# Kernel tuning notes

Measured on AMD Instinct MI355X. Metric: run time of the kernel, lower is better.

Reference implementation:

```python
import math
import jax, jax.numpy as jnp
import numpy as np

# ---- module constants (from init_kwargs) ----
B, IN, OUT, NR = 4096, 512, 512, 16
WL_MIN, WL_MAX = 1546.0e-9, 1554.0e-9
WL0 = 0.5 * (WL_MIN + WL_MAX)          # center wavelength
R_UM, NEFF, NG = 30.0, 2.34, 4.2
LOSS_DB_CM, KAPPA = 3.0, 0.2
L = 2.0 * math.pi * (R_UM * 1e-6)      # ring circumference [m]
A_AMP = 10.0 ** (-LOSS_DB_CM * (L * 100.0) / 20.0)  # single-pass amplitude
R_T = math.sqrt(1.0 - KAPPA)           # through-coupling amplitude


def _ring_neffs():
    # per-ring effective index detuning from phase_offsets (as in __init__)
    offsets = jnp.linspace(-math.pi, math.pi, NR, dtype=jnp.float32)
    return jnp.float32(NEFF) + offsets * jnp.float32(WL0 / (2.0 * math.pi * L))  # [NR]


def _evaluate_basis(x):
    # wavelengths driven by (clamped) inputs: [B, IN]
    wl = WL_MIN + 0.5 * (jnp.clip(x, -1.0, 1.0) + 1.0) * (WL_MAX - WL_MIN)
    wl = wl[..., None]                                  # [B, IN, 1]
    neff_r = _ring_neffs()                              # [NR]
    # first-order dispersion around WL0 (waveguide with neff, ng)
    neff_wl = neff_r - (wl - WL0) * (NG - neff_r) / WL0  # [B, IN, NR]
    phi = (2.0 * math.pi * L) * neff_wl / wl            # round-trip phase
    c = jnp.cos(phi)
    # all-pass ring power throughput (analytic transfer function)
    num = A_AMP * A_AMP - 2.0 * R_T * A_AMP * c + R_T * R_T
    den = 1.0 - 2.0 * R_T * A_AMP * c + (R_T * A_AMP) ** 2
    return num / den                                    # [B, IN, NR]


def setup_inputs() -> dict:
    key = jax.random.key(0)
    k1, k2, k3 = jax.random.split(key, 3)
    x = jax.random.normal(k1, (B, IN), dtype=jnp.float32)
    coeffs = jax.random.normal(k2, (IN, OUT, NR), dtype=jnp.float32) * 0.05
    base_weight = jax.random.normal(k3, (IN, OUT), dtype=jnp.float32) * 0.05
    return {"x": x, "coeffs": coeffs, "base_weight": base_weight}


def reference(x, coeffs, base_weight):
    basis = _evaluate_basis(x)                          # [B, IN, NR]
    basis_out = jnp.einsum('bin,ion->bo', basis, coeffs)  # [B, OUT]
    residual = x @ base_weight                          # [B, OUT]
    kl = jnp.zeros((1,), dtype=x.dtype)                 # non-variational path
    return (basis_out + residual, kl)
```

## Files before the change

kernel.cpp:

```cpp
#include <hip/hip_runtime.h>
#include <hip/hip_bf16.h>
#include <cmath>
#include <cstdint>

#define Bsz   4096
#define INsz  512
#define OUTsz 512
#define NRING 16
#define KTOT  8704
#define SPLITK 4
#define NPH   34

using short8 = __attribute__((ext_vector_type(8))) short;
using f32x4  = __attribute__((ext_vector_type(4))) float;

struct RC {
  float Cr[NRING];
  float Snr[NRING];
  float K2, SQ, pad0, pad1;
};

__device__ __forceinline__ unsigned short f2bf(float f) {
  __hip_bfloat16 h = __float2bfloat16(f);
  return *reinterpret_cast<unsigned short*>(&h);
}
__device__ __forceinline__ float fastrcp(float x) {
#if __has_builtin(__builtin_amdgcn_rcpf)
  return __builtin_amdgcn_rcpf(x);
#else
  return 1.0f / x;
#endif
}
__device__ __forceinline__ float fastfract(float x) {
#if __has_builtin(__builtin_amdgcn_fractf)
  return __builtin_amdgcn_fractf(x);
#else
  return x - floorf(x);
#endif
}
__device__ __forceinline__ float cos2pi(float fr) {
#if __has_builtin(__builtin_amdgcn_cosf)
  return __builtin_amdgcn_cosf(fr);
#else
  return __cosf(fr * 6.28318530717958647692f);
#endif
}
__device__ __forceinline__ float sin2pi(float fr) {
#if __has_builtin(__builtin_amdgcn_sinf)
  return __builtin_amdgcn_sinf(fr);
#else
  return __sinf(fr * 6.28318530717958647692f);
#endif
}

__device__ __forceinline__ void gl_lds16(const void* g, void* l) {
  __builtin_amdgcn_global_load_lds(
      (const __attribute__((address_space(1))) void*)g,
      (__attribute__((address_space(3))) void*)l, 16, 0, 0);
}

__global__ __launch_bounds__(512) void pack_b_kernel(
    const float* __restrict__ coeffs, const float* __restrict__ bw,
    unsigned short* __restrict__ Bt, float* __restrict__ bias, float PQ) {
  __shared__ float red[8];
  const int o = blockIdx.x;
  const int i = threadIdx.x;
  const float* cp = coeffs + ((size_t)i * OUTsz + o) * NRING;
  unsigned short* row = Bt + (size_t)o * KTOT + i;
  float s = 0.0f;
#pragma unroll
  for (int j = 0; j < 4; ++j) {
    f32x4 v = *reinterpret_cast<const f32x4*>(cp + j * 4);
#pragma unroll
    for (int e = 0; e < 4; ++e) {
      const int n = j * 4 + e;
      s += v[e];
      row[(size_t)n * INsz] = f2bf(PQ * v[e]);
    }
  }
  row[(size_t)NRING * INsz] = f2bf(bw[(size_t)i * OUTsz + o]);
#pragma unroll
  for (int off = 32; off > 0; off >>= 1) s += __shfl_down(s, off);
  const int w = i >> 6;
  if ((i & 63) == 0) red[w] = s;
  __syncthreads();
  if (i == 0) {
    float t = 0.0f;
#pragma unroll
    for (int k = 0; k < 8; ++k) t += red[k];
    bias[o] = t;
  }
}

__global__ __launch_bounds__(512) void gemm_fused_kernel(
    const float* __restrict__ x, const unsigned short* __restrict__ Bt,
    float* __restrict__ part, RC rc) {
  extern __shared__ char smem[];
  char* smA = smem;
  char* smB = smem + 32768;
  const int tid  = threadIdx.x;
  const int lane = tid & 63;
  const int w    = tid >> 6;
  const int bid  = blockIdx.x;
  const int cbks = bid & 7;
  const int rb   = bid >> 3;
  const int cb   = cbks & 1, ks = cbks >> 1;
  const int brow = rb * 128, bcol = cb * 256;

  const int r  = tid & 127;
  const int q4 = tid >> 7;
  const int wb0 = r * 128 + (((q4 * 2 + 0) ^ (r & 7)) * 16);
  const int wb1 = r * 128 + (((q4 * 2 + 1) ^ (r & 7)) * 16);

  const int cg = (lane & 7) ^ ((lane >> 3) & 7);
  const unsigned short* gb0 = Bt + (size_t)(bcol + w * 8 + (lane >> 3)) * KTOT + cg * 8;

  const int wr = w >> 2, wc = w & 3;
  const int l7 = lane & 7;
  const int rowA = wr * 64 + (lane & 15);
  const int rowB = wc * 64 + (lane & 15);

  float xr[32], cth[32], sth[32];
  const float* gx = x + (size_t)(brow + r) * INsz + ks * 128 + q4 * 16;
#pragma unroll
  for (int h = 0; h < 2; ++h)
#pragma unroll
    for (int j = 0; j < 4; ++j) {
      f32x4 v = *reinterpret_cast<const f32x4*>(gx + h * 64 + j * 4);
#pragma unroll
      for (int e = 0; e < 4; ++e) xr[h * 16 + j * 4 + e] = v[e];
    }
#pragma unroll
  for (int c = 0; c < 32; ++c) {
    float xc = fminf(fmaxf(xr[c], -1.0f), 1.0f);
    float wl = __builtin_fmaf(xc, 4.0e-9f, 1550.0e-9f);
    float hh = rc.K2 * xc * fastrcp(wl);
    float fr = fastfract(hh);
    cth[c] = cos2pi(fr);
    sth[c] = sin2pi(fr);
  }

  auto STAGE = [&](int p) {
    const int is = (p >= 17) ? 1 : 0, n = p - 17 * is;
    const size_t koff = (size_t)(n * 512 + ks * 128 + is * 64);
    char* ldst = smB + (p % 3) * 32768 + w * 1024;
    const unsigned short* src = gb0 + koff;
#pragma unroll
    for (int iss = 0; iss < 4; ++iss)
      gl_lds16(src + (size_t)iss * 64 * KTOT, ldst + iss * 8192);
  };
  auto GENA = [&](int p) {
    const int is = (p >= 17) ? 1 : 0, n = p - 17 * is;
    char* dst = smA + (p & 1) * 16384;
    if (n < NRING) {
      const float Crn = rc.Cr[n], Snn = rc.Snr[n];
#pragma unroll
      for (int g = 0; g < 2; ++g) {
        short8 wv;
#pragma unroll
        for (int e = 0; e < 8; ++e) {
          const int c = is * 16 + g * 8 + e;
          float cph = __builtin_fmaf(cth[c], Crn, sth[c] * Snn);
          wv[e] = (short)f2bf(fastrcp(cph + rc.SQ));
        }
        *reinterpret_cast<short8*>(dst + (g ? wb1 : wb0)) = wv;
      }
    } else {
#pragma unroll
      for (int g = 0; g < 2; ++g) {
        short8 wv;
#pragma unroll
        for (int e = 0; e < 8; ++e) wv[e] = (short)f2bf(xr[is * 16 + g * 8 + e]);
        *reinterpret_cast<short8*>(dst + (g ? wb1 : wb0)) = wv;
      }
    }
  };

  f32x4 acc[4][4];
#pragma unroll
  for (int m = 0; m < 4; ++m)
#pragma unroll
    for (int q = 0; q < 4; ++q) acc[m][q] = (f32x4){0.f, 0.f, 0.f, 0.f};

  STAGE(0); STAGE(1);
  GENA(0);
  asm volatile("s_waitcnt vmcnt(4) lgkmcnt(0)" ::: "memory");
  __builtin_amdgcn_s_barrier();
  __builtin_amdgcn_sched_barrier(0);

#pragma unroll
  for (int p = 0; p < NPH; ++p) {
    if (p + 2 < NPH) STAGE(p + 2);
    const char* bA = smA + (p & 1) * 16384;
    const char* bB = smB + (p % 3) * 32768;
    short8 af[2][4], bfr[2][4];
#pragma unroll
    for (int kk = 0; kk < 2; ++kk) {
      const int oct = (((lane >> 4) + kk * 4) ^ l7) * 16;
#pragma unroll
      for (int m = 0; m < 4; ++m)
        af[kk][m] = *reinterpret_cast<const short8*>(bA + (rowA + m * 16) * 128 + oct);
#pragma unroll
      for (int q = 0; q < 4; ++q)
        bfr[kk][q] = *reinterpret_cast<const short8*>(bB + (rowB + q * 16) * 128 + oct);
    }
    if (p + 1 < NPH) GENA(p + 1);
    __builtin_amdgcn_s_setprio(1);
#pragma unroll
    for (int kk = 0; kk < 2; ++kk)
#pragma unroll
      for (int m = 0; m < 4; ++m)
#pragma unroll
        for (int q = 0; q < 4; ++q)
          acc[m][q] = __builtin_amdgcn_mfma_f32_16x16x32_bf16(af[kk][m], bfr[kk][q], acc[m][q], 0, 0, 0);
    __builtin_amdgcn_s_setprio(0);
    if (p + 1 < NPH) {
      if (p + 2 < NPH) {
        asm volatile("s_waitcnt vmcnt(4) lgkmcnt(0)" ::: "memory");
      } else {
        asm volatile("s_waitcnt vmcnt(0) lgkmcnt(0)" ::: "memory");
      }
      __builtin_amdgcn_s_barrier();
      __builtin_amdgcn_sched_barrier(0);
    }
  }

  float* po = part + (size_t)ks * ((size_t)Bsz * OUTsz);
  const int r0 = brow + wr * 64 + ((lane >> 4) * 4);
  const int c0 = bcol + wc * 64 + (lane & 15);
#pragma unroll
  for (int m = 0; m < 4; ++m)
#pragma unroll
    for (int q = 0; q < 4; ++q)
#pragma unroll
      for (int e = 0; e < 4; ++e)
        po[(size_t)(r0 + m * 16 + e) * OUTsz + (c0 + q * 16)] = acc[m][q][e];
}

__global__ __launch_bounds__(256) void reduce_kernel(
    const f32x4* __restrict__ part, const f32x4* __restrict__ bias,
    float* __restrict__ out) {
  const size_t idx = (size_t)blockIdx.x * 256 + threadIdx.x;
  const size_t stride = (size_t)Bsz * OUTsz / 4;
  f32x4 v = part[idx] + part[idx + stride] + part[idx + 2 * stride] + part[idx + 3 * stride];
  v = v + bias[idx & 127];
  reinterpret_cast<f32x4*>(out)[idx] = v;
  if (idx == 0) out[(size_t)Bsz * OUTsz] = 0.0f;
}

extern "C" void kernel_launch(void* const* d_in, const int* in_sizes, int n_in,
                              void* d_out, int out_size, void* d_ws, size_t ws_size,
                              hipStream_t stream) {
  const float* x      = (const float*)d_in[0];
  const float* coeffs = (const float*)d_in[1];
  const float* bw     = (const float*)d_in[2];
  float* out = (float*)d_out;

  unsigned short* Bt = (unsigned short*)d_ws;
  float* part = (float*)((char*)d_ws + (size_t)OUTsz * KTOT * 2);
  float* bias = (float*)((char*)d_ws + (size_t)OUTsz * KTOT * 2
                                     + (size_t)SPLITK * Bsz * OUTsz * 4);

  RC rc;
  float PQ;
  {
    const double PI  = 3.14159265358979323846;
    const double Lc  = 2.0 * PI * 30.0e-6;
    const double WL0 = 1550.0e-9;
    const double NG  = 4.2;
    const double Aamp = pow(10.0, -3.0 * (Lc * 100.0) / 20.0);
    const double Rt2  = 0.8;
    const double Rt   = sqrt(Rt2);
    for (int rr = 0; rr < NRING; ++rr) {
      double off  = -PI + rr * (2.0 * PI / 15.0);
      double neff = 2.34 + off * WL0 / (2.0 * PI * Lc);
      double rev0 = (Lc / WL0) * neff;
      rc.Cr[rr]  = (float)cos(2.0 * PI * rev0);
      rc.Snr[rr] = (float)(-sin(2.0 * PI * rev0));
    }
    const double qn = -2.0 * Rt * Aamp;
    const double s  = 1.0 + Rt2 * Aamp * Aamp;
    const double P  = -(1.0 - Aamp * Aamp) * (1.0 - Rt2);
    rc.K2 = (float)(-4.0e-9 * Lc * NG / WL0);
    rc.SQ = (float)(s / qn);
    rc.pad0 = rc.pad1 = 0.f;
    PQ = (float)(P / qn);
  }

  hipFuncSetAttribute(reinterpret_cast<const void*>(gemm_fused_kernel),
                      hipFuncAttributeMaxDynamicSharedMemorySize, 131072);

  hipLaunchKernelGGL(pack_b_kernel, dim3(OUTsz), dim3(512), 0, stream,
                     coeffs, bw, Bt, bias, PQ);
  hipLaunchKernelGGL(gemm_fused_kernel, dim3(256), dim3(512), 131072, stream,
                     x, Bt, part, rc);
  hipLaunchKernelGGL(reduce_kernel, dim3((Bsz * OUTsz / 4) / 256), dim3(256), 0, stream,
                     (const f32x4*)part, (const f32x4*)bias, out);
}
```

Measured before the change: 62.25 us.

## Halve GEMM column tile to 128 and double grid size for occupancy

Shrinks each block's output tile from 128x256 to 128x128, so the grid doubles to 512 blocks, B-operand LDS staging halves, and dynamic shared memory drops to 80 KB. Per-thread register use is cut by computing trig values for only half the K columns at a time (the second half at phase 16) and pre-converting x to bf16 once. It also adds a launch-bounds occupancy hint. The intent is more active blocks per CU and better load balance across the 256 CUs. In exchange, every block now regenerates the A-operand basis, so that transcendental work is duplicated across twice as many column blocks.

```diff
diff --git a/kernel.cpp b/kernel.cpp
--- a/kernel.cpp
+++ b/kernel.cpp
@@ -92,7 +92,7 @@
   }
 }
 
-__global__ __launch_bounds__(512) void gemm_fused_kernel(
+__global__ __launch_bounds__(512, 4) void gemm_fused_kernel(
     const float* __restrict__ x, const unsigned short* __restrict__ Bt,
     float* __restrict__ part, RC rc) {
   extern __shared__ char smem[];
@@ -102,10 +102,10 @@
   const int lane = tid & 63;
   const int w    = tid >> 6;
   const int bid  = blockIdx.x;
-  const int cbks = bid & 7;
-  const int rb   = bid >> 3;
-  const int cb   = cbks & 1, ks = cbks >> 1;
-  const int brow = rb * 128, bcol = cb * 256;
+  const int combo = bid & 15;
+  const int rb   = bid >> 4;
+  const int cb   = combo & 3, ks = combo >> 2;
+  const int brow = rb * 128, bcol = cb * 128;
 
   const int r  = tid & 127;
   const int q4 = tid >> 7;
@@ -118,36 +118,43 @@
   const int wr = w >> 2, wc = w & 3;
   const int l7 = lane & 7;
   const int rowA = wr * 64 + (lane & 15);
-  const int rowB = wc * 64 + (lane & 15);
-
-  float xr[32], cth[32], sth[32];
+  const int rowB = wc * 32 + (lane & 15);
+
+  float xf0[16], xf1[16], cth[16], sth[16];
+  short8 xbf0a, xbf0b, xbf1a, xbf1b;
   const float* gx = x + (size_t)(brow + r) * INsz + ks * 128 + q4 * 16;
 #pragma unroll
-  for (int h = 0; h < 2; ++h)
-#pragma unroll
-    for (int j = 0; j < 4; ++j) {
-      f32x4 v = *reinterpret_cast<const f32x4*>(gx + h * 64 + j * 4);
-#pragma unroll
-      for (int e = 0; e < 4; ++e) xr[h * 16 + j * 4 + e] = v[e];
-    }
-#pragma unroll
-  for (int c = 0; c < 32; ++c) {
-    float xc = fminf(fmaxf(xr[c], -1.0f), 1.0f);
-    float wl = __builtin_fmaf(xc, 4.0e-9f, 1550.0e-9f);
-    float hh = rc.K2 * xc * fastrcp(wl);
-    float fr = fastfract(hh);
-    cth[c] = cos2pi(fr);
-    sth[c] = sin2pi(fr);
-  }
+  for (int j = 0; j < 4; ++j) {
+    f32x4 v0 = *reinterpret_cast<const f32x4*>(gx + j * 4);
+    f32x4 v1 = *reinterpret_cast<const f32x4*>(gx + 64 + j * 4);
+#pragma unroll
+    for (int e = 0; e < 4; ++e) { xf0[j * 4 + e] = v0[e]; xf1[j * 4 + e] = v1[e]; }
+  }
+#pragma unroll
+  for (int c = 0; c < 8; ++c) {
+    xbf0a[c] = (short)f2bf(xf0[c]);     xbf0b[c] = (short)f2bf(xf0[c + 8]);
+    xbf1a[c] = (short)f2bf(xf1[c]);     xbf1b[c] = (short)f2bf(xf1[c + 8]);
+  }
+  auto TRIG = [&](const float* xf) {
+#pragma unroll
+    for (int c = 0; c < 16; ++c) {
+      float xc = fminf(fmaxf(xf[c], -1.0f), 1.0f);
+      float wl = __builtin_fmaf(xc, 4.0e-9f, 1550.0e-9f);
+      float hh = rc.K2 * xc * fastrcp(wl);
+      float fr = fastfract(hh);
+      cth[c] = cos2pi(fr);
+      sth[c] = sin2pi(fr);
+    }
+  };
+  TRIG(xf0);
 
   auto STAGE = [&](int p) {
     const int is = (p >= 17) ? 1 : 0, n = p - 17 * is;
     const size_t koff = (size_t)(n * 512 + ks * 128 + is * 64);
-    char* ldst = smB + (p % 3) * 32768 + w * 1024;
+    char* ldst = smB + (p % 3) * 16384 + w * 1024;
     const unsigned short* src = gb0 + koff;
-#pragma unroll
-    for (int iss = 0; iss < 4; ++iss)
-      gl_lds16(src + (size_t)iss * 64 * KTOT, ldst + iss * 8192);
+    gl_lds16(src, ldst);
+    gl_lds16(src + (size_t)64 * KTOT, ldst + 8192);
   };
   auto GENA = [&](int p) {
     const int is = (p >= 17) ? 1 : 0, n = p - 17 * is;
@@ -159,41 +166,36 @@
         short8 wv;
 #pragma unroll
         for (int e = 0; e < 8; ++e) {
-          const int c = is * 16 + g * 8 + e;
-          float cph = __builtin_fmaf(cth[c], Crn, sth[c] * Snn);
+          float cph = __builtin_fmaf(cth[g * 8 + e], Crn, sth[g * 8 + e] * Snn);
           wv[e] = (short)f2bf(fastrcp(cph + rc.SQ));
         }
         *reinterpret_cast<short8*>(dst + (g ? wb1 : wb0)) = wv;
       }
     } else {
-#pragma unroll
-      for (int g = 0; g < 2; ++g) {
-        short8 wv;
-#pragma unroll
-        for (int e = 0; e < 8; ++e) wv[e] = (short)f2bf(xr[is * 16 + g * 8 + e]);
-        *reinterpret_cast<short8*>(dst + (g ? wb1 : wb0)) = wv;
-      }
+      *reinterpret_cast<short8*>(dst + wb0) = is ? xbf1a : xbf0a;
+      *reinterpret_cast<short8*>(dst + wb1) = is ? xbf1b : xbf0b;
     }
   };
 
-  f32x4 acc[4][4];
+  f32x4 acc[4][2];
 #pragma unroll
   for (int m = 0; m < 4; ++m)
 #pragma unroll
-    for (int q = 0; q < 4; ++q) acc[m][q] = (f32x4){0.f, 0.f, 0.f, 0.f};
+    for (int q = 0; q < 2; ++q) acc[m][q] = (f32x4){0.f, 0.f, 0.f, 0.f};
 
   STAGE(0); STAGE(1);
   GENA(0);
-  asm volatile("s_waitcnt vmcnt(4) lgkmcnt(0)" ::: "memory");
+  asm volatile("s_waitcnt vmcnt(2) lgkmcnt(0)" ::: "memory");
   __builtin_amdgcn_s_barrier();
   __builtin_amdgcn_sched_barrier(0);
 
 #pragma unroll
   for (int p = 0; p < NPH; ++p) {
     if (p + 2 < NPH) STAGE(p + 2);
+    if (p == 16) TRIG(xf1);
     const char* bA = smA + (p & 1) * 16384;
-    const char* bB = smB + (p % 3) * 32768;
-    short8 af[2][4], bfr[2][4];
+    const char* bB = smB + (p % 3) * 16384;
+    short8 af[2][4], bfr[2][2];
 #pragma unroll
     for (int kk = 0; kk < 2; ++kk) {
       const int oct = (((lane >> 4) + kk * 4) ^ l7) * 16;
@@ -201,7 +203,7 @@
       for (int m = 0; m < 4; ++m)
         af[kk][m] = *reinterpret_cast<const short8*>(bA + (rowA + m * 16) * 128 + oct);
 #pragma unroll
-      for (int q = 0; q < 4; ++q)
+      for (int q = 0; q < 2; ++q)
         bfr[kk][q] = *reinterpret_cast<const short8*>(bB + (rowB + q * 16) * 128 + oct);
     }
     if (p + 1 < NPH) GENA(p + 1);
@@ -211,12 +213,12 @@
 #pragma unroll
       for (int m = 0; m < 4; ++m)
 #pragma unroll
-        for (int q = 0; q < 4; ++q)
+        for (int q = 0; q < 2; ++q)
           acc[m][q] = __builtin_amdgcn_mfma_f32_16x16x32_bf16(af[kk][m], bfr[kk][q], acc[m][q], 0, 0, 0);
     __builtin_amdgcn_s_setprio(0);
     if (p + 1 < NPH) {
       if (p + 2 < NPH) {
-        asm volatile("s_waitcnt vmcnt(4) lgkmcnt(0)" ::: "memory");
+        asm volatile("s_waitcnt vmcnt(2) lgkmcnt(0)" ::: "memory");
       } else {
         asm volatile("s_waitcnt vmcnt(0) lgkmcnt(0)" ::: "memory");
       }
@@ -227,11 +229,11 @@
 
   float* po = part + (size_t)ks * ((size_t)Bsz * OUTsz);
   const int r0 = brow + wr * 64 + ((lane >> 4) * 4);
-  const int c0 = bcol + wc * 64 + (lane & 15);
+  const int c0 = bcol + wc * 32 + (lane & 15);
 #pragma unroll
   for (int m = 0; m < 4; ++m)
 #pragma unroll
-    for (int q = 0; q < 4; ++q)
+    for (int q = 0; q < 2; ++q)
 #pragma unroll
       for (int e = 0; e < 4; ++e)
         po[(size_t)(r0 + m * 16 + e) * OUTsz + (c0 + q * 16)] = acc[m][q][e];
@@ -288,11 +290,11 @@
   }
 
   hipFuncSetAttribute(reinterpret_cast<const void*>(gemm_fused_kernel),
-                      hipFuncAttributeMaxDynamicSharedMemorySize, 131072);
+                      hipFuncAttributeMaxDynamicSharedMemorySize, 81920);
 
   hipLaunchKernelGGL(pack_b_kernel, dim3(OUTsz), dim3(512), 0, stream,
                      coeffs, bw, Bt, bias, PQ);
-  hipLaunchKernelGGL(gemm_fused_kernel, dim3(256), dim3(512), 131072, stream,
+  hipLaunchKernelGGL(gemm_fused_kernel, dim3(512), dim3(512), 81920, stream,
                      x, Bt, part, rc);
   hipLaunchKernelGGL(reduce_kernel, dim3((Bsz * OUTsz / 4) / 256), dim3(256), 0, stream,
                      (const f32x4*)part, (const f32x4*)bias, out);
```

After: 86.62 us. 39.2% more time.

## Split each phase into two ping-pong MFMA halves with extra barriers and lower register use

Applied to the files above, without the earlier changes.

Each pipeline phase now runs as two half-K sub-steps. Each sub-step loads its LDS fragments, passes a barrier and runs 16 MFMAs, and the A-tile generation and global staging are placed between the halves. Register pressure drops because only 16 cos/sin values are kept live (the second half is recomputed at phase 16), and the bf16 copies of x are precomputed once. The aim is better overlap of MFMA with LDS reads and ALU generation and possibly higher occupancy, at the cost of extra barriers per phase.

```diff
diff --git a/kernel.cpp b/kernel.cpp
--- a/kernel.cpp
+++ b/kernel.cpp
@@ -120,25 +120,33 @@
   const int rowA = wr * 64 + (lane & 15);
   const int rowB = wc * 64 + (lane & 15);
 
-  float xr[32], cth[32], sth[32];
+  float xf0[16], xf1[16], cth[16], sth[16];
+  short8 xbf0a, xbf0b, xbf1a, xbf1b;
   const float* gx = x + (size_t)(brow + r) * INsz + ks * 128 + q4 * 16;
 #pragma unroll
-  for (int h = 0; h < 2; ++h)
-#pragma unroll
-    for (int j = 0; j < 4; ++j) {
-      f32x4 v = *reinterpret_cast<const f32x4*>(gx + h * 64 + j * 4);
-#pragma unroll
-      for (int e = 0; e < 4; ++e) xr[h * 16 + j * 4 + e] = v[e];
-    }
-#pragma unroll
-  for (int c = 0; c < 32; ++c) {
-    float xc = fminf(fmaxf(xr[c], -1.0f), 1.0f);
-    float wl = __builtin_fmaf(xc, 4.0e-9f, 1550.0e-9f);
-    float hh = rc.K2 * xc * fastrcp(wl);
-    float fr = fastfract(hh);
-    cth[c] = cos2pi(fr);
-    sth[c] = sin2pi(fr);
-  }
+  for (int j = 0; j < 4; ++j) {
+    f32x4 v0 = *reinterpret_cast<const f32x4*>(gx + j * 4);
+    f32x4 v1 = *reinterpret_cast<const f32x4*>(gx + 64 + j * 4);
+#pragma unroll
+    for (int e = 0; e < 4; ++e) { xf0[j * 4 + e] = v0[e]; xf1[j * 4 + e] = v1[e]; }
+  }
+#pragma unroll
+  for (int c = 0; c < 8; ++c) {
+    xbf0a[c] = (short)f2bf(xf0[c]);     xbf0b[c] = (short)f2bf(xf0[c + 8]);
+    xbf1a[c] = (short)f2bf(xf1[c]);     xbf1b[c] = (short)f2bf(xf1[c + 8]);
+  }
+  auto TRIG = [&](const float* xf) {
+#pragma unroll
+    for (int c = 0; c < 16; ++c) {
+      float xc = fminf(fmaxf(xf[c], -1.0f), 1.0f);
+      float wl = __builtin_fmaf(xc, 4.0e-9f, 1550.0e-9f);
+      float hh = rc.K2 * xc * fastrcp(wl);
+      float fr = fastfract(hh);
+      cth[c] = cos2pi(fr);
+      sth[c] = sin2pi(fr);
+    }
+  };
+  TRIG(xf0);
 
   auto STAGE = [&](int p) {
     const int is = (p >= 17) ? 1 : 0, n = p - 17 * is;
@@ -159,20 +167,14 @@
         short8 wv;
 #pragma unroll
         for (int e = 0; e < 8; ++e) {
-          const int c = is * 16 + g * 8 + e;
-          float cph = __builtin_fmaf(cth[c], Crn, sth[c] * Snn);
+          float cph = __builtin_fmaf(cth[g * 8 + e], Crn, sth[g * 8 + e] * Snn);
           wv[e] = (short)f2bf(fastrcp(cph + rc.SQ));
         }
         *reinterpret_cast<short8*>(dst + (g ? wb1 : wb0)) = wv;
       }
     } else {
-#pragma unroll
-      for (int g = 0; g < 2; ++g) {
-        short8 wv;
-#pragma unroll
-        for (int e = 0; e < 8; ++e) wv[e] = (short)f2bf(xr[is * 16 + g * 8 + e]);
-        *reinterpret_cast<short8*>(dst + (g ? wb1 : wb0)) = wv;
-      }
+      *reinterpret_cast<short8*>(dst + wb0) = is ? xbf1a : xbf0a;
+      *reinterpret_cast<short8*>(dst + wb1) = is ? xbf1b : xbf0b;
     }
   };
 
@@ -190,35 +192,56 @@
 
 #pragma unroll
   for (int p = 0; p < NPH; ++p) {
-    if (p + 2 < NPH) STAGE(p + 2);
     const char* bA = smA + (p & 1) * 16384;
     const char* bB = smB + (p % 3) * 32768;
-    short8 af[2][4], bfr[2][4];
-#pragma unroll
-    for (int kk = 0; kk < 2; ++kk) {
-      const int oct = (((lane >> 4) + kk * 4) ^ l7) * 16;
+    short8 af[4], bfr[4];
+    {
+      const int oct = ((lane >> 4) ^ l7) * 16;
 #pragma unroll
       for (int m = 0; m < 4; ++m)
-        af[kk][m] = *reinterpret_cast<const short8*>(bA + (rowA + m * 16) * 128 + oct);
+        af[m] = *reinterpret_cast<const short8*>(bA + (rowA + m * 16) * 128 + oct);
 #pragma unroll
       for (int q = 0; q < 4; ++q)
-        bfr[kk][q] = *reinterpret_cast<const short8*>(bB + (rowB + q * 16) * 128 + oct);
-    }
+        bfr[q] = *reinterpret_cast<const short8*>(bB + (rowB + q * 16) * 128 + oct);
+    }
+    if (p + 2 < NPH) STAGE(p + 2);
+    __builtin_amdgcn_s_barrier();
+    asm volatile("s_waitcnt lgkmcnt(0)" ::: "memory");
+    __builtin_amdgcn_sched_barrier(0);
+    __builtin_amdgcn_s_setprio(1);
+#pragma unroll
+    for (int m = 0; m < 4; ++m)
+#pragma unroll
+      for (int q = 0; q < 4; ++q)
+        acc[m][q] = __builtin_amdgcn_mfma_f32_16x16x32_bf16(af[m], bfr[q], acc[m][q], 0, 0, 0);
+    __builtin_amdgcn_s_setprio(0);
+    __builtin_amdgcn_s_barrier();
+    {
+      const int oct = (((lane >> 4) + 4) ^ l7) * 16;
+#pragma unroll
+      for (int m = 0; m < 4; ++m)
+        af[m] = *reinterpret_cast<const short8*>(bA + (rowA + m * 16) * 128 + oct);
+#pragma unroll
+      for (int q = 0; q < 4; ++q)
+        bfr[q] = *reinterpret_cast<const short8*>(bB + (rowB + q * 16) * 128 + oct);
+    }
+    if (p == 16) TRIG(xf1);
     if (p + 1 < NPH) GENA(p + 1);
+    __builtin_amdgcn_s_barrier();
+    asm volatile("s_waitcnt lgkmcnt(0)" ::: "memory");
+    __builtin_amdgcn_sched_barrier(0);
     __builtin_amdgcn_s_setprio(1);
 #pragma unroll
-    for (int kk = 0; kk < 2; ++kk)
-#pragma unroll
-      for (int m = 0; m < 4; ++m)
-#pragma unroll
-        for (int q = 0; q < 4; ++q)
-          acc[m][q] = __builtin_amdgcn_mfma_f32_16x16x32_bf16(af[kk][m], bfr[kk][q], acc[m][q], 0, 0, 0);
+    for (int m = 0; m < 4; ++m)
+#pragma unroll
+      for (int q = 0; q < 4; ++q)
+        acc[m][q] = __builtin_amdgcn_mfma_f32_16x16x32_bf16(af[m], bfr[q], acc[m][q], 0, 0, 0);
     __builtin_amdgcn_s_setprio(0);
     if (p + 1 < NPH) {
       if (p + 2 < NPH) {
-        asm volatile("s_waitcnt vmcnt(4) lgkmcnt(0)" ::: "memory");
+        asm volatile("s_waitcnt vmcnt(4)" ::: "memory");
       } else {
-        asm volatile("s_waitcnt vmcnt(0) lgkmcnt(0)" ::: "memory");
+        asm volatile("s_waitcnt vmcnt(0)" ::: "memory");
       }
       __builtin_amdgcn_s_barrier();
       __builtin_amdgcn_sched_barrier(0);
```

Result: slower. 66.92 us (+7.5%).

## Warp-specialize fused GEMM into producer and MFMA consumer wavefronts

Applied to the files above, without the earlier changes.

Doubles the block to 1024 threads: eight producer waves compute the ring basis tiles into LDS and issue global-to-LDS loads of B, while eight consumer waves only read LDS and run MFMA. The aim is to take the transcendental basis generation and load issue off the MFMA waves' critical path. In exchange each block carries more waves, which raises register and occupancy pressure, and loops are no longer unrolled. Producer and consumer waves also use mixed barrier primitives whose counts must match exactly.

```diff
diff --git a/kernel.cpp b/kernel.cpp
--- a/kernel.cpp
+++ b/kernel.cpp
@@ -92,7 +92,7 @@
   }
 }
 
-__global__ __launch_bounds__(512) void gemm_fused_kernel(
+__global__ __launch_bounds__(1024) void gemm_fused_kernel(
     const float* __restrict__ x, const unsigned short* __restrict__ Bt,
     float* __restrict__ part, RC rc) {
   extern __shared__ char smem[];
@@ -102,139 +102,176 @@
   const int lane = tid & 63;
   const int w    = tid >> 6;
   const int bid  = blockIdx.x;
-  const int cbks = bid & 7;
+  const int combo = bid & 7;
   const int rb   = bid >> 3;
-  const int cb   = cbks & 1, ks = cbks >> 1;
+  const int cb   = combo & 1, ks = combo >> 1;
   const int brow = rb * 128, bcol = cb * 256;
 
-  const int r  = tid & 127;
-  const int q4 = tid >> 7;
-  const int wb0 = r * 128 + (((q4 * 2 + 0) ^ (r & 7)) * 16);
-  const int wb1 = r * 128 + (((q4 * 2 + 1) ^ (r & 7)) * 16);
-
-  const int cg = (lane & 7) ^ ((lane >> 3) & 7);
-  const unsigned short* gb0 = Bt + (size_t)(bcol + w * 8 + (lane >> 3)) * KTOT + cg * 8;
-
-  const int wr = w >> 2, wc = w & 3;
-  const int l7 = lane & 7;
-  const int rowA = wr * 64 + (lane & 15);
-  const int rowB = wc * 64 + (lane & 15);
-
-  float xr[32], cth[32], sth[32];
-  const float* gx = x + (size_t)(brow + r) * INsz + ks * 128 + q4 * 16;
-#pragma unroll
-  for (int h = 0; h < 2; ++h)
-#pragma unroll
-    for (int j = 0; j < 4; ++j) {
-      f32x4 v = *reinterpret_cast<const f32x4*>(gx + h * 64 + j * 4);
-#pragma unroll
-      for (int e = 0; e < 4; ++e) xr[h * 16 + j * 4 + e] = v[e];
-    }
-#pragma unroll
-  for (int c = 0; c < 32; ++c) {
-    float xc = fminf(fmaxf(xr[c], -1.0f), 1.0f);
-    float wl = __builtin_fmaf(xc, 4.0e-9f, 1550.0e-9f);
-    float hh = rc.K2 * xc * fastrcp(wl);
-    float fr = fastfract(hh);
-    cth[c] = cos2pi(fr);
-    sth[c] = sin2pi(fr);
-  }
-
-  auto STAGE = [&](int p) {
-    const int is = (p >= 17) ? 1 : 0, n = p - 17 * is;
-    const size_t koff = (size_t)(n * 512 + ks * 128 + is * 64);
-    char* ldst = smB + (p % 3) * 32768 + w * 1024;
-    const unsigned short* src = gb0 + koff;
-#pragma unroll
-    for (int iss = 0; iss < 4; ++iss)
-      gl_lds16(src + (size_t)iss * 64 * KTOT, ldst + iss * 8192);
-  };
-  auto GENA = [&](int p) {
-    const int is = (p >= 17) ? 1 : 0, n = p - 17 * is;
-    char* dst = smA + (p & 1) * 16384;
-    if (n < NRING) {
-      const float Crn = rc.Cr[n], Snn = rc.Snr[n];
-#pragma unroll
-      for (int g = 0; g < 2; ++g) {
-        short8 wv;
-#pragma unroll
-        for (int e = 0; e < 8; ++e) {
-          const int c = is * 16 + g * 8 + e;
-          float cph = __builtin_fmaf(cth[c], Crn, sth[c] * Snn);
-          wv[e] = (short)f2bf(fastrcp(cph + rc.SQ));
+  if (w < 8) {
+    const int r  = tid & 127;
+    const int q4 = tid >> 7;
+    const int wb0 = r * 128 + (((q4 * 2 + 0) ^ (r & 7)) * 16);
+    const int wb1 = r * 128 + (((q4 * 2 + 1) ^ (r & 7)) * 16);
+    const int cg = (lane & 7) ^ ((lane >> 3) & 7);
+    const unsigned short* gb0 = Bt + (size_t)(bcol + w * 8 + (lane >> 3)) * KTOT
+                                   + ks * 128 + cg * 8;
+
+    auto STAGE = [&](int p, int slot) {
+      const int is = (p >= 17) ? 1 : 0;
+      const int n  = p - 17 * is;
+      char* ldst = smB + slot * 32768 + w * 1024;
+      const unsigned short* src = gb0 + n * 512 + is * 64;
+#pragma unroll
+      for (int iss = 0; iss < 4; ++iss)
+        gl_lds16(src + (size_t)iss * 64 * KTOT, ldst + iss * 8192);
+    };
+
+    float xf0[16], xf1[16];
+    {
+      const float* gx = x + (size_t)(brow + r) * INsz + ks * 128 + q4 * 16;
+#pragma unroll
+      for (int j = 0; j < 4; ++j) {
+        f32x4 v0 = *reinterpret_cast<const f32x4*>(gx + j * 4);
+        f32x4 v1 = *reinterpret_cast<const f32x4*>(gx + 64 + j * 4);
+#pragma unroll
+        for (int e = 0; e < 4; ++e) { xf0[j*4+e] = v0[e]; xf1[j*4+e] = v1[e]; }
+      }
+    }
+    STAGE(0, 0); STAGE(1, 1);
+
+    short8 x0a, x0b, x1a, x1b;
+#pragma unroll
+    for (int c = 0; c < 8; ++c) {
+      x0a[c] = (short)f2bf(xf0[c]);   x0b[c] = (short)f2bf(xf0[c + 8]);
+      x1a[c] = (short)f2bf(xf1[c]);   x1b[c] = (short)f2bf(xf1[c + 8]);
+    }
+    float cth0[16], sth0[16], cth1[16], sth1[16];
+#pragma unroll
+    for (int c = 0; c < 16; ++c) {
+      float xc = fminf(fmaxf(xf0[c], -1.0f), 1.0f);
+      float wl = __builtin_fmaf(xc, 4.0e-9f, 1550.0e-9f);
+      float fr = fastfract(rc.K2 * xc * fastrcp(wl));
+      cth0[c] = cos2pi(fr);  sth0[c] = sin2pi(fr);
+    }
+#pragma unroll
+    for (int c = 0; c < 16; ++c) {
+      float xc = fminf(fmaxf(xf1[c], -1.0f), 1.0f);
+      float wl = __builtin_fmaf(xc, 4.0e-9f, 1550.0e-9f);
+      float fr = fastfract(rc.K2 * xc * fastrcp(wl));
+      cth1[c] = cos2pi(fr);  sth1[c] = sin2pi(fr);
+    }
+
+    auto GEN = [&](char* dst, int ring, const float (&ct)[16], const float (&st)[16],
+                   short8 xa, short8 xb, float Crn, float Snn) {
+      if (ring < NRING) {
+#pragma unroll
+        for (int g = 0; g < 2; ++g) {
+          short8 wv;
+#pragma unroll
+          for (int e = 0; e < 8; ++e) {
+            float cph = __builtin_fmaf(ct[g * 8 + e], Crn, st[g * 8 + e] * Snn);
+            wv[e] = (short)f2bf(fastrcp(cph + rc.SQ));
+          }
+          *reinterpret_cast<short8*>(dst + (g ? wb1 : wb0)) = wv;
         }
-        *reinterpret_cast<short8*>(dst + (g ? wb1 : wb0)) = wv;
+      } else {
+        *reinterpret_cast<short8*>(dst + wb0) = xa;
+        *reinterpret_cast<short8*>(dst + wb1) = xb;
       }
-    } else {
-#pragma unroll
-      for (int g = 0; g < 2; ++g) {
-        short8 wv;
-#pragma unroll
-        for (int e = 0; e < 8; ++e) wv[e] = (short)f2bf(xr[is * 16 + g * 8 + e]);
-        *reinterpret_cast<short8*>(dst + (g ? wb1 : wb0)) = wv;
-      }
-    }
-  };
-
-  f32x4 acc[4][4];
-#pragma unroll
-  for (int m = 0; m < 4; ++m)
-#pragma unroll
-    for (int q = 0; q < 4; ++q) acc[m][q] = (f32x4){0.f, 0.f, 0.f, 0.f};
-
-  STAGE(0); STAGE(1);
-  GENA(0);
-  asm volatile("s_waitcnt vmcnt(4) lgkmcnt(0)" ::: "memory");
-  __builtin_amdgcn_s_barrier();
-  __builtin_amdgcn_sched_barrier(0);
-
-#pragma unroll
-  for (int p = 0; p < NPH; ++p) {
-    if (p + 2 < NPH) STAGE(p + 2);
-    const char* bA = smA + (p & 1) * 16384;
-    const char* bB = smB + (p % 3) * 32768;
-    short8 af[2][4], bfr[2][4];
-#pragma unroll
-    for (int kk = 0; kk < 2; ++kk) {
-      const int oct = (((lane >> 4) + kk * 4) ^ l7) * 16;
-#pragma unroll
-      for (int m = 0; m < 4; ++m)
-        af[kk][m] = *reinterpret_cast<const short8*>(bA + (rowA + m * 16) * 128 + oct);
-#pragma unroll
-      for (int q = 0; q < 4; ++q)
-        bfr[kk][q] = *reinterpret_cast<const short8*>(bB + (rowB + q * 16) * 128 + oct);
-    }
-    if (p + 1 < NPH) GENA(p + 1);
-    __builtin_amdgcn_s_setprio(1);
-#pragma unroll
-    for (int kk = 0; kk < 2; ++kk)
-#pragma unroll
-      for (int m = 0; m < 4; ++m)
-#pragma unroll
-        for (int q = 0; q < 4; ++q)
-          acc[m][q] = __builtin_amdgcn_mfma_f32_16x16x32_bf16(af[kk][m], bfr[kk][q], acc[m][q], 0, 0, 0);
-    __builtin_amdgcn_s_setprio(0);
-    if (p + 1 < NPH) {
+    };
+
+    GEN(smA, 0, cth0, sth0, x0a, x0b, rc.Cr[0], rc.Snr[0]);
+    asm volatile("s_waitcnt vmcnt(4) lgkmcnt(0)" ::: "memory");
+    __builtin_amdgcn_s_barrier();
+    __builtin_amdgcn_sched_barrier(0);
+
+    int slotS = 2;
+    int bufG  = 1;
+#pragma unroll 1
+    for (int p = 0; p < 16; ++p) {
+      const int ring = p + 1;
+      GEN(smA + bufG * 16384, ring, cth0, sth0, x0a, x0b,
+          rc.Cr[ring & 15], rc.Snr[ring & 15]);
+      STAGE(p + 2, slotS);
+      slotS = (slotS == 2) ? 0 : slotS + 1;
+      bufG ^= 1;
+      asm volatile("s_waitcnt vmcnt(4) lgkmcnt(0)" ::: "memory");
+      __builtin_amdgcn_s_barrier();
+      __builtin_amdgcn_sched_barrier(0);
+    }
+#pragma unroll 1
+    for (int p = 16; p < 33; ++p) {
+      const int ring = p - 16;
+      GEN(smA + bufG * 16384, ring, cth1, sth1, x1a, x1b,
+          rc.Cr[ring & 15], rc.Snr[ring & 15]);
       if (p + 2 < NPH) {
+        STAGE(p + 2, slotS);
+        slotS = (slotS == 2) ? 0 : slotS + 1;
         asm volatile("s_waitcnt vmcnt(4) lgkmcnt(0)" ::: "memory");
       } else {
         asm volatile("s_waitcnt vmcnt(0) lgkmcnt(0)" ::: "memory");
       }
+      bufG ^= 1;
       __builtin_amdgcn_s_barrier();
       __builtin_amdgcn_sched_barrier(0);
     }
+    __builtin_amdgcn_s_barrier();
+  } else {
+    const int cw = w - 8;
+    const int wr = cw >> 2, wc = cw & 3;
+    const int l7 = lane & 7;
+    const int rowA = wr * 64 + (lane & 15);
+    const int rowB = wc * 64 + (lane & 15);
+    const int oct0 = (((lane >> 4) + 0) ^ l7) * 16;
+    const int oct1 = (((lane >> 4) + 4) ^ l7) * 16;
+
+    f32x4 acc[4][4];
+#pragma unroll
+    for (int m = 0; m < 4; ++m)
+#pragma unroll
+      for (int q = 0; q < 4; ++q) acc[m][q] = (f32x4){0.f, 0.f, 0.f, 0.f};
+
+    __syncthreads();
+
+    int slotB = 0, bufA = 0;
+#pragma unroll 1
+    for (int p = 0; p < NPH; ++p) {
+      const char* bA = smA + bufA * 16384;
+      const char* bB = smB + slotB * 32768;
+#pragma unroll
+      for (int kk = 0; kk < 2; ++kk) {
+        const int oct = kk ? oct1 : oct0;
+        short8 af[4], bf[4];
+#pragma unroll
+        for (int m = 0; m < 4; ++m)
+          af[m] = *reinterpret_cast<const short8*>(bA + (rowA + m * 16) * 128 + oct);
+#pragma unroll
+        for (int q = 0; q < 4; ++q)
+          bf[q] = *reinterpret_cast<const short8*>(bB + (rowB + q * 16) * 128 + oct);
+        __builtin_amdgcn_s_setprio(1);
+#pragma unroll
+        for (int m = 0; m < 4; ++m)
+#pragma unroll
+          for (int q = 0; q < 4; ++q)
+            acc[m][q] = __builtin_amdgcn_mfma_f32_16x16x32_bf16(af[m], bf[q], acc[m][q], 0, 0, 0);
+        __builtin_amdgcn_s_setprio(0);
+      }
+      bufA ^= 1;
+      slotB = (slotB == 2) ? 0 : slotB + 1;
+      __syncthreads();
+    }
+
+    float* po = part + (size_t)ks * ((size_t)Bsz * OUTsz);
+    const int r0 = brow + wr * 64 + ((lane >> 4) * 4);
+    const int c0 = bcol + wc * 64 + (lane & 15);
+#pragma unroll
+    for (int m = 0; m < 4; ++m)
+#pragma unroll
+      for (int q = 0; q < 4; ++q)
+#pragma unroll
+        for (int e = 0; e < 4; ++e)
+          po[(size_t)(r0 + m * 16 + e) * OUTsz + (c0 + q * 16)] = acc[m][q][e];
   }
-
-  float* po = part + (size_t)ks * ((size_t)Bsz * OUTsz);
-  const int r0 = brow + wr * 64 + ((lane >> 4) * 4);
-  const int c0 = bcol + wc * 64 + (lane & 15);
-#pragma unroll
-  for (int m = 0; m < 4; ++m)
-#pragma unroll
-    for (int q = 0; q < 4; ++q)
-#pragma unroll
-      for (int e = 0; e < 4; ++e)
-        po[(size_t)(r0 + m * 16 + e) * OUTsz + (c0 + q * 16)] = acc[m][q][e];
 }
 
 __global__ __launch_bounds__(256) void reduce_kernel(
@@ -292,7 +329,7 @@
 
   hipLaunchKernelGGL(pack_b_kernel, dim3(OUTsz), dim3(512), 0, stream,
                      coeffs, bw, Bt, bias, PQ);
-  hipLaunchKernelGGL(gemm_fused_kernel, dim3(256), dim3(512), 131072, stream,
+  hipLaunchKernelGGL(gemm_fused_kernel, dim3(256), dim3(1024), 131072, stream,
                      x, Bt, part, rc);
   hipLaunchKernelGGL(reduce_kernel, dim3((Bsz * OUTsz / 4) / 256), dim3(256), 0, stream,
                      (const f32x4*)part, (const f32x4*)bias, out);
```

Measured after the change: 64.54 us. 1.04x slower.
